# Optimization experiments

Hardware: AMD Instinct MI355X
Metric: run time of the kernel (lower is better)

## Reference

```python
import jax, jax.numpy as jnp
import numpy as np
import math

B, C, L = 16, 512, 1024

def setup_inputs() -> dict:
    key = jax.random.key(0)
    kq, kk, kv = jax.random.split(key, 3)
    q = jax.random.normal(kq, (B, C, L), dtype=jnp.float32)
    k = jax.random.normal(kk, (B, C, L), dtype=jnp.float32)
    v = jax.random.normal(kv, (B, C, L), dtype=jnp.float32)
    return {"q": q, "k": k, "v": v}

def reference(q, k, v):
    # q, k, v: (b, c, l)
    b, c, l = q.shape
    # score[b, i, j] = sum_c k[b, c, i] * q[b, c, j]  -> (b, l, l)
    score = jnp.einsum('bci,bcj->bij', k, q) / math.sqrt(l)
    # Faithful to torch nn.Softmax() with dim=None on a 3D tensor:
    # torch's _get_softmax_dim picks dim=1 for ndim not in (0,1,3); ndim==3 -> dim=0.
    score = jax.nn.softmax(score, axis=0)
    # out[b, c, j] = sum_i v[b, c, i] * score[b, i, j]  -> (b, c, l)
    out = jnp.einsum('bci,bij->bcj', v, score)
    return out
```

## Files before the change

kernel.cpp:

```cpp
#include <hip/hip_runtime.h>
#include <hip/hip_bf16.h>


#define LN 1024
#define CC 512
#define BN 16

typedef __attribute__((ext_vector_type(8))) short bf16x8;
typedef __attribute__((ext_vector_type(4))) float f32x4;

static __device__ __forceinline__ unsigned short f2bf(float x) {
  union { float f; unsigned u; } un; un.f = x;
  unsigned r = un.u + 0x7fffu + ((un.u >> 16) & 1u);
  return (unsigned short)(r >> 16);
}
static __device__ __forceinline__ float bf2f(unsigned short h) {
  union { unsigned u; float f; } un; un.u = ((unsigned)h) << 16; return un.f;
}

__global__ __launch_bounds__(256) void transpose_convert(
    const float* __restrict__ q, const float* __restrict__ k,
    unsigned short* __restrict__ qT, unsigned short* __restrict__ kT) {
  __shared__ float tile[32][33];
  const int b   = blockIdx.z >> 1;
  const int mat = blockIdx.z & 1;
  const float* src = mat ? k : q;
  unsigned short* dst = mat ? kT : qT;
  const int l0 = blockIdx.x * 32, c0 = blockIdx.y * 32;
  const int t = threadIdx.x;
  const int ll = t & 31, cbase = t >> 5;
  const float* sp = src + ((size_t)b * CC + c0) * LN + l0;
#pragma unroll
  for (int r = 0; r < 4; ++r) {
    int cc = cbase + r * 8;
    tile[cc][ll] = sp[(size_t)cc * LN + ll];
  }
  __syncthreads();
  const int co = t & 31, lbase = t >> 5;
  unsigned short* dp = dst + ((size_t)b * LN + l0) * CC + c0;
#pragma unroll
  for (int r = 0; r < 4; ++r) {
    int lo = lbase + r * 8;
    dp[(size_t)lo * CC + co] = f2bf(tile[co][lo]);
  }
}

template<int KD, int LDAv, int LDBv, int LDCv, bool OBF, int NTN, int NTM, int NB>
__global__ __launch_bounds__(256, 5) void gemm_glds(
    const unsigned short* __restrict__ A, const unsigned short* __restrict__ B,
    void* __restrict__ Cv, float scale,
    size_t strideA, size_t strideB, size_t strideC) {
  __shared__ unsigned short As[2][128 * 32];
  __shared__ unsigned short Bs[2][128 * 32];

  constexpr int nwg = NTN * NTM * NB;
  const int f = blockIdx.x + NTN * (blockIdx.y + NTM * blockIdx.z);
  const int wid = (f & 7) * (nwg >> 3) + (f >> 3);
  const int tn = wid % NTN;
  const int tm = (wid / NTN) % NTM;
  const int bz = wid / (NTN * NTM);

  const unsigned short* Ab = A + (size_t)bz * strideA;
  const unsigned short* Bb = B + (size_t)bz * strideB;
  const int t = threadIdx.x, w = t >> 6, l = t & 63;
  const int wr = w >> 1, wc = w & 1;
  const int lr = l & 15, lks = l >> 4;

  f32x4 acc[4][4];
#pragma unroll
  for (int m = 0; m < 4; ++m)
#pragma unroll
    for (int n = 0; n < 4; ++n) acc[m][n] = (f32x4){0.f, 0.f, 0.f, 0.f};

  const int srow = t >> 2;
  const int sslot = t & 3;

  auto STAGE = [&](int buf, int step) {
    const int c0 = step * 32;
#pragma unroll
    for (int qq = 0; qq < 2; ++qq) {
      const int row = qq * 64 + srow;
      const unsigned short* ga =
          Ab + (size_t)(tm * 128 + row) * LDAv + c0 + ((sslot ^ ((row >> 1) & 3)) * 8);
      __builtin_amdgcn_global_load_lds(
          (const __attribute__((address_space(1))) void*)ga,
          (__attribute__((address_space(3))) void*)&As[buf][qq * 2048 + t * 8],
          16, 0, 0);
    }
#pragma unroll
    for (int qq = 0; qq < 2; ++qq) {
      const int row = qq * 64 + srow;
      const unsigned short* gb =
          Bb + (size_t)(tn * 128 + row) * LDBv + c0 + ((sslot ^ ((row >> 1) & 3)) * 8);
      __builtin_amdgcn_global_load_lds(
          (const __attribute__((address_space(1))) void*)gb,
          (__attribute__((address_space(3))) void*)&Bs[buf][qq * 2048 + t * 8],
          16, 0, 0);
    }
  };

  STAGE(0, 0);
  __syncthreads();

  const int NSTEP = KD / 32;
  int cur = 0;
#pragma unroll 1
  for (int step = 0; step < NSTEP; ++step) {
    if (step + 1 < NSTEP) STAGE(cur ^ 1, step + 1);
    bf16x8 af[4], bfr[4];
#pragma unroll
    for (int m = 0; m < 4; ++m) {
      const int r = wr * 64 + m * 16 + lr;
      const int slot = lks ^ ((r >> 1) & 3);
      af[m] = *(const bf16x8*)(&As[cur][r * 32 + slot * 8]);
    }
#pragma unroll
    for (int n = 0; n < 4; ++n) {
      const int r = wc * 64 + n * 16 + lr;
      const int slot = lks ^ ((r >> 1) & 3);
      bfr[n] = *(const bf16x8*)(&Bs[cur][r * 32 + slot * 8]);
    }
#pragma unroll
    for (int m = 0; m < 4; ++m)
#pragma unroll
      for (int n = 0; n < 4; ++n)
        acc[m][n] = __builtin_amdgcn_mfma_f32_16x16x32_bf16(af[m], bfr[n], acc[m][n], 0, 0, 0);
    __syncthreads();
    cur ^= 1;
  }

#pragma unroll
  for (int m = 0; m < 4; ++m)
#pragma unroll
    for (int n = 0; n < 4; ++n)
#pragma unroll
      for (int r = 0; r < 4; ++r) {
        const int row = tm * 128 + wr * 64 + m * 16 + (l >> 4) * 4 + r;
        const int col = tn * 128 + wc * 64 + n * 16 + lr;
        if (OBF) {
          ((unsigned short*)Cv)[bz * strideC + (size_t)row * LDCv + col] =
              f2bf(acc[m][n][r] * scale);
        } else {
          ((float*)Cv)[bz * strideC + (size_t)row * LDCv + col] = acc[m][n][r] * scale;
        }
      }
}

__global__ __launch_bounds__(256) void convert_v(
    const float* __restrict__ v, unsigned short* __restrict__ vB) {
  const size_t i8 = (size_t)blockIdx.x * 256 + threadIdx.x;
  const float4 a = *(const float4*)(v + i8 * 8);
  const float4 b = *(const float4*)(v + i8 * 8 + 4);
  bf16x8 o;
  o[0] = (short)f2bf(a.x); o[1] = (short)f2bf(a.y);
  o[2] = (short)f2bf(a.z); o[3] = (short)f2bf(a.w);
  o[4] = (short)f2bf(b.x); o[5] = (short)f2bf(b.y);
  o[6] = (short)f2bf(b.z); o[7] = (short)f2bf(b.w);
  *(bf16x8*)(vB + i8 * 8) = o;
}

__global__ __launch_bounds__(256) void softmax_b(unsigned short* __restrict__ SP) {
  const size_t off = ((size_t)blockIdx.x * 256 + threadIdx.x) * 8;
  bf16x8 s[BN];
#pragma unroll
  for (int b = 0; b < BN; ++b)
    s[b] = *(const bf16x8*)(SP + (size_t)b * (LN * LN) + off);
#pragma unroll
  for (int e = 0; e < 8; ++e) {
    float vv[BN];
#pragma unroll
    for (int b = 0; b < BN; ++b) vv[b] = bf2f((unsigned short)s[b][e]);
    float m = vv[0];
#pragma unroll
    for (int b = 1; b < BN; ++b) m = fmaxf(m, vv[b]);
    float tt[BN], sum = 0.f;
#pragma unroll
    for (int b = 0; b < BN; ++b) { tt[b] = __expf(vv[b] - m); sum += tt[b]; }
    const float inv = 1.f / sum;
#pragma unroll
    for (int b = 0; b < BN; ++b) s[b][e] = (short)f2bf(tt[b] * inv);
  }
#pragma unroll
  for (int b = 0; b < BN; ++b)
    *(bf16x8*)(SP + (size_t)b * (LN * LN) + off) = s[b];
}

extern "C" void kernel_launch(void* const* d_in, const int* in_sizes, int n_in,
                              void* d_out, int out_size, void* d_ws, size_t ws_size,
                              hipStream_t stream) {
  const float* q = (const float*)d_in[0];
  const float* k = (const float*)d_in[1];
  const float* v = (const float*)d_in[2];
  float* out = (float*)d_out;

  unsigned short* qT = (unsigned short*)d_ws;
  unsigned short* kT = qT + (size_t)BN * LN * CC;
  unsigned short* SP = kT + (size_t)BN * LN * CC;
  unsigned short* vB = qT;

  transpose_convert<<<dim3(LN / 32, CC / 32, BN * 2), 256, 0, stream>>>(q, k, qT, kT);
  gemm_glds<512, 512, 512, 1024, true, 8, 8, BN><<<dim3(8, 8, BN), 256, 0, stream>>>(
      qT, kT, (void*)SP, 0.03125f,
      (size_t)LN * CC, (size_t)LN * CC, (size_t)LN * LN);
  convert_v<<<dim3((BN * CC * LN) / 8 / 256), 256, 0, stream>>>(v, vB);
  softmax_b<<<dim3((LN * LN) / 8 / 256), 256, 0, stream>>>(SP);
  gemm_glds<1024, 1024, 1024, 1024, false, 8, 4, BN><<<dim3(8, 4, BN), 256, 0, stream>>>(
      vB, SP, (void*)out, 1.0f,
      (size_t)CC * LN, (size_t)LN * LN, (size_t)CC * LN);
}
```

Measured before the change: 95.41 us.

## Use 256x256-tile 8-wave ping-pong GEMM for the score computation

Adds a new GEMM kernel with 512 threads and 256x256 output tiles over a BK=64 double buffer. The mainloop is split into four barrier-separated phases that interleave LDS fragment reads, async global-to-LDS prefetches and MFMA bursts, with raised wave priority during math. It replaces only the first (score) GEMM, aiming for more data reuse per tile and better overlap of loads with compute. The cost is that the grid shrinks from 1024 to 256 workgroups, and the hand-placed waitcnt/barrier sequencing is fragile.

```diff
diff --git a/kernel.cpp b/kernel.cpp
--- a/kernel.cpp
+++ b/kernel.cpp
@@ -46,6 +46,171 @@
 }
 
 template<int KD, int LDAv, int LDBv, int LDCv, bool OBF, int NTN, int NTM, int NB>
+__global__ __launch_bounds__(512, 2) void gemm_8ph(
+    const unsigned short* __restrict__ A, const unsigned short* __restrict__ B,
+    void* __restrict__ Cv, float scale,
+    size_t strideA, size_t strideB, size_t strideC) {
+  __shared__ unsigned short As[2][2][128 * 64];
+  __shared__ unsigned short Bs[2][2][128 * 64];
+
+  constexpr int nwg = NTN * NTM * NB;
+  const int f = blockIdx.x + NTN * (blockIdx.y + NTM * blockIdx.z);
+  const int wid = (f & 7) * (nwg >> 3) + (f >> 3);
+  const int tn = wid % NTN;
+  const int tm = (wid / NTN) % NTM;
+  const int bz = wid / (NTN * NTM);
+
+  const unsigned short* Ab = A + (size_t)bz * strideA;
+  const unsigned short* Bb = B + (size_t)bz * strideB;
+
+  const int t = threadIdx.x;
+  const int w = t >> 6, l = t & 63;
+  const int wr = w >> 2;
+  const int wc = w & 3;
+  const int lr = l & 15, lks = l >> 4;
+
+  f32x4 acc[8][4];
+#pragma unroll
+  for (int m = 0; m < 8; ++m)
+#pragma unroll
+    for (int n = 0; n < 4; ++n) acc[m][n] = (f32x4){0.f, 0.f, 0.f, 0.f};
+
+  const int NSTEP = KD / 64;
+
+  auto SA = [&](int tile, int h) {
+    const int buf = tile & 1, c0 = tile * 64;
+#pragma unroll
+    for (int j = 0; j < 2; ++j) {
+      const int s = j * 512 + t, r = s >> 3, pu = s & 7;
+      const unsigned short* g =
+          Ab + (size_t)(tm * 256 + h * 128 + r) * LDAv + c0 + ((pu ^ (r & 7)) * 8);
+      __builtin_amdgcn_global_load_lds(
+          (const __attribute__((address_space(1))) void*)g,
+          (__attribute__((address_space(3))) void*)&As[buf][h][s * 8], 16, 0, 0);
+    }
+  };
+  auto SB = [&](int tile, int h) {
+    const int buf = tile & 1, c0 = tile * 64;
+#pragma unroll
+    for (int j = 0; j < 2; ++j) {
+      const int s = j * 512 + t, r = s >> 3, pu = s & 7;
+      const unsigned short* g =
+          Bb + (size_t)(tn * 256 + h * 128 + r) * LDBv + c0 + ((pu ^ (r & 7)) * 8);
+      __builtin_amdgcn_global_load_lds(
+          (const __attribute__((address_space(1))) void*)g,
+          (__attribute__((address_space(3))) void*)&Bs[buf][h][s * 8], 16, 0, 0);
+    }
+  };
+  auto LA = [&](int buf, int rloc, int kk) -> bf16x8 {
+    return *(const bf16x8*)(&As[buf][wr][rloc * 64 + (((kk * 4 + lks) ^ (rloc & 7)) * 8)]);
+  };
+  auto LB = [&](int buf, int rloc, int kk) -> bf16x8 {
+    return *(const bf16x8*)(&Bs[buf][wc >> 1][rloc * 64 + (((kk * 4 + lks) ^ (rloc & 7)) * 8)]);
+  };
+
+  SB(0, 0); SB(0, 1); SA(0, 0); SA(0, 1);
+  if (NSTEP > 1) { SB(1, 0); SB(1, 1); }
+  asm volatile("s_waitcnt vmcnt(4)\n\ts_barrier" ::: "memory");
+
+  bf16x8 a[4][2], b[4][2];
+  const int brow = (wc & 1) * 64;
+
+#pragma unroll 1
+  for (int T = 0; T < NSTEP; ++T) {
+    const int buf = T & 1;
+#pragma unroll
+    for (int m = 0; m < 4; ++m) {
+      a[m][0] = LA(buf, m * 16 + lr, 0);
+      a[m][1] = LA(buf, m * 16 + lr, 1);
+    }
+#pragma unroll
+    for (int n = 0; n < 2; ++n) {
+      b[n][0] = LB(buf, brow + n * 16 + lr, 0);
+      b[n][1] = LB(buf, brow + n * 16 + lr, 1);
+    }
+    if (T + 1 < NSTEP) SA(T + 1, 0);
+    asm volatile("s_barrier" ::: "memory");
+    __builtin_amdgcn_s_setprio(1);
+#pragma unroll
+    for (int m = 0; m < 4; ++m)
+#pragma unroll
+      for (int n = 0; n < 2; ++n) {
+        acc[m][n] = __builtin_amdgcn_mfma_f32_16x16x32_bf16(a[m][0], b[n][0], acc[m][n], 0, 0, 0);
+        acc[m][n] = __builtin_amdgcn_mfma_f32_16x16x32_bf16(a[m][1], b[n][1], acc[m][n], 0, 0, 0);
+      }
+    __builtin_amdgcn_s_setprio(0);
+    asm volatile("s_barrier" ::: "memory");
+#pragma unroll
+    for (int n = 2; n < 4; ++n) {
+      b[n][0] = LB(buf, brow + n * 16 + lr, 0);
+      b[n][1] = LB(buf, brow + n * 16 + lr, 1);
+    }
+    if (T + 1 < NSTEP) SA(T + 1, 1);
+    asm volatile("s_barrier" ::: "memory");
+    __builtin_amdgcn_s_setprio(1);
+#pragma unroll
+    for (int m = 0; m < 4; ++m)
+#pragma unroll
+      for (int n = 2; n < 4; ++n) {
+        acc[m][n] = __builtin_amdgcn_mfma_f32_16x16x32_bf16(a[m][0], b[n][0], acc[m][n], 0, 0, 0);
+        acc[m][n] = __builtin_amdgcn_mfma_f32_16x16x32_bf16(a[m][1], b[n][1], acc[m][n], 0, 0, 0);
+      }
+    __builtin_amdgcn_s_setprio(0);
+    asm volatile("s_barrier" ::: "memory");
+#pragma unroll
+    for (int m = 0; m < 4; ++m) {
+      a[m][0] = LA(buf, 64 + m * 16 + lr, 0);
+      a[m][1] = LA(buf, 64 + m * 16 + lr, 1);
+    }
+    if (T + 2 < NSTEP) SB(T + 2, 0);
+    asm volatile("s_barrier" ::: "memory");
+    __builtin_amdgcn_s_setprio(1);
+#pragma unroll
+    for (int m = 0; m < 4; ++m)
+#pragma unroll
+      for (int n = 0; n < 2; ++n) {
+        acc[m + 4][n] = __builtin_amdgcn_mfma_f32_16x16x32_bf16(a[m][0], b[n][0], acc[m + 4][n], 0, 0, 0);
+        acc[m + 4][n] = __builtin_amdgcn_mfma_f32_16x16x32_bf16(a[m][1], b[n][1], acc[m + 4][n], 0, 0, 0);
+      }
+    __builtin_amdgcn_s_setprio(0);
+    asm volatile("s_barrier" ::: "memory");
+    if (T + 2 < NSTEP) SB(T + 2, 1);
+    if (T < NSTEP - 2) {
+      asm volatile("s_waitcnt vmcnt(4)" ::: "memory");
+    } else if (T == NSTEP - 2) {
+      asm volatile("s_waitcnt vmcnt(0)" ::: "memory");
+    }
+    asm volatile("s_barrier" ::: "memory");
+    __builtin_amdgcn_s_setprio(1);
+#pragma unroll
+    for (int m = 0; m < 4; ++m)
+#pragma unroll
+      for (int n = 2; n < 4; ++n) {
+        acc[m + 4][n] = __builtin_amdgcn_mfma_f32_16x16x32_bf16(a[m][0], b[n][0], acc[m + 4][n], 0, 0, 0);
+        acc[m + 4][n] = __builtin_amdgcn_mfma_f32_16x16x32_bf16(a[m][1], b[n][1], acc[m + 4][n], 0, 0, 0);
+      }
+    __builtin_amdgcn_s_setprio(0);
+    asm volatile("s_barrier" ::: "memory");
+  }
+
+#pragma unroll
+  for (int m = 0; m < 8; ++m)
+#pragma unroll
+    for (int n = 0; n < 4; ++n)
+#pragma unroll
+      for (int r = 0; r < 4; ++r) {
+        const int row = tm * 256 + wr * 128 + m * 16 + (l >> 4) * 4 + r;
+        const int col = tn * 256 + wc * 64 + n * 16 + lr;
+        if (OBF) {
+          ((unsigned short*)Cv)[bz * strideC + (size_t)row * LDCv + col] =
+              f2bf(acc[m][n][r] * scale);
+        } else {
+          ((float*)Cv)[bz * strideC + (size_t)row * LDCv + col] = acc[m][n][r] * scale;
+        }
+      }
+}
+
+template<int KD, int LDAv, int LDBv, int LDCv, bool OBF, int NTN, int NTM, int NB>
 __global__ __launch_bounds__(256, 5) void gemm_glds(
     const unsigned short* __restrict__ A, const unsigned short* __restrict__ B,
     void* __restrict__ Cv, float scale,
@@ -199,7 +364,7 @@
   unsigned short* vB = qT;
 
   transpose_convert<<<dim3(LN / 32, CC / 32, BN * 2), 256, 0, stream>>>(q, k, qT, kT);
-  gemm_glds<512, 512, 512, 1024, true, 8, 8, BN><<<dim3(8, 8, BN), 256, 0, stream>>>(
+  gemm_8ph<512, 512, 512, 1024, true, 4, 4, BN><<<dim3(4, 4, BN), 512, 0, stream>>>(
       qT, kT, (void*)SP, 0.03125f,
       (size_t)LN * CC, (size_t)LN * CC, (size_t)LN * LN);
   convert_v<<<dim3((BN * CC * LN) / 8 / 256), 256, 0, stream>>>(v, vB);
```

Result: faster. 92.83 us (-2.7%).

## Widen transpose tiles with vector I/O and process two batches per score-GEMM block

Applied to the files above, without the earlier changes.

The transpose kernel now uses 64x64 tiles, reading with float4 loads and writing 8-wide bf16 vector stores, so global traffic is coalesced and vectorized. The first GEMM now gives each workgroup two consecutive batches. Its K loop runs continuously across both batches, writing out the first batch's tile midway. This halves the grid to 512 blocks and keeps the pipeline full across the batch boundary. Fewer blocks may reduce occupancy balance, and the mid-loop store adds latency inside the pipelined loop.

```diff
diff --git a/kernel.cpp b/kernel.cpp
--- a/kernel.cpp
+++ b/kernel.cpp
@@ -18,31 +18,139 @@
   union { unsigned u; float f; } un; un.u = ((unsigned)h) << 16; return un.f;
 }
 
-__global__ __launch_bounds__(256) void transpose_convert(
+__global__ __launch_bounds__(256) void transpose_convert64(
     const float* __restrict__ q, const float* __restrict__ k,
     unsigned short* __restrict__ qT, unsigned short* __restrict__ kT) {
-  __shared__ float tile[32][33];
-  const int b   = blockIdx.z >> 1;
-  const int mat = blockIdx.z & 1;
+  __shared__ float tile[64][65];
+  const int b = blockIdx.z >> 1, mat = blockIdx.z & 1;
   const float* src = mat ? k : q;
   unsigned short* dst = mat ? kT : qT;
-  const int l0 = blockIdx.x * 32, c0 = blockIdx.y * 32;
+  const int l0 = blockIdx.x * 64, c0 = blockIdx.y * 64;
   const int t = threadIdx.x;
-  const int ll = t & 31, cbase = t >> 5;
-  const float* sp = src + ((size_t)b * CC + c0) * LN + l0;
-#pragma unroll
-  for (int r = 0; r < 4; ++r) {
-    int cc = cbase + r * 8;
-    tile[cc][ll] = sp[(size_t)cc * LN + ll];
+  const int lv = (t & 15) * 4, cr = t >> 4;
+#pragma unroll
+  for (int p = 0; p < 4; ++p) {
+    const int c = cr + p * 16;
+    const float4 v4 = *(const float4*)(src + ((size_t)b * CC + c0 + c) * LN + l0 + lv);
+    tile[c][lv] = v4.x; tile[c][lv + 1] = v4.y;
+    tile[c][lv + 2] = v4.z; tile[c][lv + 3] = v4.w;
   }
   __syncthreads();
-  const int co = t & 31, lbase = t >> 5;
-  unsigned short* dp = dst + ((size_t)b * LN + l0) * CC + c0;
-#pragma unroll
-  for (int r = 0; r < 4; ++r) {
-    int lo = lbase + r * 8;
-    dp[(size_t)lo * CC + co] = f2bf(tile[co][lo]);
-  }
+  const int c8 = (t & 7) * 8, lw = t >> 3;
+#pragma unroll
+  for (int p = 0; p < 2; ++p) {
+    const int l = lw + p * 32;
+    bf16x8 o;
+#pragma unroll
+    for (int i = 0; i < 8; ++i) o[i] = (short)f2bf(tile[c8 + i][l]);
+    *(bf16x8*)(dst + ((size_t)b * LN + l0 + l) * CC + c0 + c8) = o;
+  }
+}
+
+template<int LDAv, int LDBv, int LDCv, int NTN, int NTM, int NBQ>
+__global__ __launch_bounds__(256, 5) void gemm_2b(
+    const unsigned short* __restrict__ A, const unsigned short* __restrict__ B,
+    unsigned short* __restrict__ C, float scale,
+    size_t strideA, size_t strideB, size_t strideC) {
+  __shared__ unsigned short As[2][128 * 32];
+  __shared__ unsigned short Bs[2][128 * 32];
+
+  constexpr int nwg = NTN * NTM * NBQ;
+  const int f = blockIdx.x + NTN * (blockIdx.y + NTM * blockIdx.z);
+  const int wid = (f & 7) * (nwg >> 3) + (f >> 3);
+  const int tn = wid % NTN;
+  const int tm = (wid / NTN) % NTM;
+  const int bz0 = (wid / (NTN * NTM)) * 2;
+
+  const int t = threadIdx.x, w = t >> 6, l = t & 63;
+  const int wr = w >> 1, wc = w & 1;
+  const int lr = l & 15, lks = l >> 4;
+
+  f32x4 acc[4][4];
+#pragma unroll
+  for (int m = 0; m < 4; ++m)
+#pragma unroll
+    for (int n = 0; n < 4; ++n) acc[m][n] = (f32x4){0.f, 0.f, 0.f, 0.f};
+
+  const int srow = t >> 2;
+  const int sslot = t & 3;
+
+  auto STAGE = [&](int buf, int s) {
+    const int bb = s >> 4, c0 = (s & 15) * 32;
+    const unsigned short* Abb = A + (size_t)(bz0 + bb) * strideA;
+    const unsigned short* Bbb = B + (size_t)(bz0 + bb) * strideB;
+#pragma unroll
+    for (int qq = 0; qq < 2; ++qq) {
+      const int row = qq * 64 + srow;
+      const unsigned short* ga =
+          Abb + (size_t)(tm * 128 + row) * LDAv + c0 + ((sslot ^ ((row >> 1) & 3)) * 8);
+      __builtin_amdgcn_global_load_lds(
+          (const __attribute__((address_space(1))) void*)ga,
+          (__attribute__((address_space(3))) void*)&As[buf][qq * 2048 + t * 8],
+          16, 0, 0);
+    }
+#pragma unroll
+    for (int qq = 0; qq < 2; ++qq) {
+      const int row = qq * 64 + srow;
+      const unsigned short* gb =
+          Bbb + (size_t)(tn * 128 + row) * LDBv + c0 + ((sslot ^ ((row >> 1) & 3)) * 8);
+      __builtin_amdgcn_global_load_lds(
+          (const __attribute__((address_space(1))) void*)gb,
+          (__attribute__((address_space(3))) void*)&Bs[buf][qq * 2048 + t * 8],
+          16, 0, 0);
+    }
+  };
+
+  auto WRITEC = [&](int bb) {
+#pragma unroll
+    for (int m = 0; m < 4; ++m)
+#pragma unroll
+      for (int n = 0; n < 4; ++n)
+#pragma unroll
+        for (int r = 0; r < 4; ++r) {
+          const int row = tm * 128 + wr * 64 + m * 16 + (l >> 4) * 4 + r;
+          const int col = tn * 128 + wc * 64 + n * 16 + lr;
+          C[(size_t)(bz0 + bb) * strideC + (size_t)row * LDCv + col] =
+              f2bf(acc[m][n][r] * scale);
+        }
+  };
+
+  STAGE(0, 0);
+  __syncthreads();
+
+  int cur = 0;
+#pragma unroll 1
+  for (int s = 0; s < 32; ++s) {
+    if (s + 1 < 32) STAGE(cur ^ 1, s + 1);
+    bf16x8 af[4], bfr[4];
+#pragma unroll
+    for (int m = 0; m < 4; ++m) {
+      const int r = wr * 64 + m * 16 + lr;
+      const int slot = lks ^ ((r >> 1) & 3);
+      af[m] = *(const bf16x8*)(&As[cur][r * 32 + slot * 8]);
+    }
+#pragma unroll
+    for (int n = 0; n < 4; ++n) {
+      const int r = wc * 64 + n * 16 + lr;
+      const int slot = lks ^ ((r >> 1) & 3);
+      bfr[n] = *(const bf16x8*)(&Bs[cur][r * 32 + slot * 8]);
+    }
+#pragma unroll
+    for (int m = 0; m < 4; ++m)
+#pragma unroll
+      for (int n = 0; n < 4; ++n)
+        acc[m][n] = __builtin_amdgcn_mfma_f32_16x16x32_bf16(af[m], bfr[n], acc[m][n], 0, 0, 0);
+    if (s == 15) {
+      WRITEC(0);
+#pragma unroll
+      for (int m = 0; m < 4; ++m)
+#pragma unroll
+        for (int n = 0; n < 4; ++n) acc[m][n] = (f32x4){0.f, 0.f, 0.f, 0.f};
+    }
+    __syncthreads();
+    cur ^= 1;
+  }
+  WRITEC(1);
 }
 
 template<int KD, int LDAv, int LDBv, int LDCv, bool OBF, int NTN, int NTM, int NB>
@@ -198,9 +306,9 @@
   unsigned short* SP = kT + (size_t)BN * LN * CC;
   unsigned short* vB = qT;
 
-  transpose_convert<<<dim3(LN / 32, CC / 32, BN * 2), 256, 0, stream>>>(q, k, qT, kT);
-  gemm_glds<512, 512, 512, 1024, true, 8, 8, BN><<<dim3(8, 8, BN), 256, 0, stream>>>(
-      qT, kT, (void*)SP, 0.03125f,
+  transpose_convert64<<<dim3(LN / 64, CC / 64, BN * 2), 256, 0, stream>>>(q, k, qT, kT);
+  gemm_2b<512, 512, 1024, 8, 8, 8><<<dim3(8, 8, 8), 256, 0, stream>>>(
+      qT, kT, SP, 0.03125f,
       (size_t)LN * CC, (size_t)LN * CC, (size_t)LN * LN);
   convert_v<<<dim3((BN * CC * LN) / 8 / 256), 256, 0, stream>>>(v, vB);
   softmax_b<<<dim3((LN * LN) / 8 / 256), 256, 0, stream>>>(SP);
```

Measured after the change: 134.7 us. 41.2% more time.
